# Kernel optimization log

Hardware: AMD Instinct MI355X
Metric: run time of the kernel (lower is better)

The kernel has to match this reference:

```python
import jax, jax.numpy as jnp
import numpy as np

N_SRC, N_DST, E = 10000, 10000, 640000
S, T, O, H = 128, 128, 128, 4
D = O // H


def setup_inputs() -> dict:
    key = jax.random.key(0)
    ks = jax.random.split(key, 12)
    f = lambda k, shape, fan: jax.random.normal(k, shape, dtype=jnp.float32) / np.float32(np.sqrt(fan))
    return {
        "x_src": jax.random.normal(ks[0], (N_SRC, S), dtype=jnp.float32),
        "x_dst": jax.random.normal(ks[1], (N_DST, T), dtype=jnp.float32),
        "W_pred1": f(ks[2], (S, T), T),
        "b_pred1": jnp.zeros((S,), jnp.float32),
        "W_pred2": f(ks[3], (S, S), S),
        "b_pred2": jnp.zeros((S,), jnp.float32),
        "W_res": f(ks[4], (H * D, S), S),
        "W_src": f(ks[5], (H * D, S), S),
        "W_dst": f(ks[6], (H * D, T), T),
        "att_src": jax.random.normal(ks[7], (1, H, D), dtype=jnp.float32) * 0.01,
        "att_dst": jax.random.normal(ks[8], (1, H, D), dtype=jnp.float32) * 0.01,
        "W_self": f(ks[9], (H * D, T), T),
        "b_self": jnp.zeros((H * D,), jnp.float32),
        "edge_src": jax.random.randint(ks[10], (E,), 0, N_SRC),
        "edge_dst": jax.random.randint(ks[11], (E,), 0, N_DST),
        "num_dst": N_DST,
    }


def reference(x_src, x_dst, W_pred1, b_pred1, W_pred2, b_pred2, W_res, W_src, W_dst,
              att_src, att_dst, W_self, b_self, edge_src, edge_dst, num_dst):
    h, d = att_src.shape[1], att_src.shape[2]
    # residual prediction path: pred_mlp(x_dst) = Lin2(ReLU(Lin1(x_dst)))
    pred = jax.nn.relu(x_dst @ W_pred1.T + b_pred1) @ W_pred2.T + b_pred2  # [Ndst,S]
    residual = x_src[edge_src] - pred[edge_dst]                            # [E,S]
    # per-node attention logits (equivalent to gather-then-dot, cheaper)
    a_s = ((x_src @ W_src.T).reshape(-1, h, d) * att_src).sum(-1)          # [Nsrc,H]
    a_d = ((x_dst @ W_dst.T).reshape(-1, h, d) * att_dst).sum(-1)          # [Ndst,H]
    alpha = jax.nn.leaky_relu(a_s[edge_src] + a_d[edge_dst], 0.2)          # [E,H]
    # edge softmax over incoming edges of each destination node
    amax = jax.ops.segment_max(alpha, edge_dst, num_segments=num_dst)      # [Ndst,H]
    ex = jnp.exp(alpha - amax[edge_dst])
    denom = jax.ops.segment_sum(ex, edge_dst, num_segments=num_dst)
    alpha = ex / (denom[edge_dst] + 1e-16)                                 # [E,H]
    # attention-weighted aggregation of transformed residuals
    msg = (residual @ W_res.T).reshape(-1, h, d) * alpha[:, :, None]       # [E,H,D]
    agg = jax.ops.segment_sum(msg.reshape(-1, h * d), edge_dst, num_segments=num_dst)
    return agg + x_dst @ W_self.T + b_self                                 # [Ndst,H*D]
```

## Files before the change

kernel.cpp:

```cpp
#include <hip/hip_runtime.h>
#include <hip/hip_bf16.h>

#define LEAKY 0.2f
#define CAP 160
#define CAPB 8192
#define CHUNK 2048
#define GSTRIDE 32

#define FMA4(A, S, V) do { (A).x += (S)*(V).x; (A).y += (S)*(V).y; (A).z += (S)*(V).z; (A).w += (S)*(V).w; } while (0)

typedef __attribute__((ext_vector_type(8))) short bf16x8;
typedef __attribute__((ext_vector_type(4))) float f32x4;

struct GemmJob {
  const float* X; const float* W; const float* B; float* Y;
  int M; int relu; int bf16out;
  const float* vvec;
  float* aout;
};

__device__ __forceinline__ unsigned short f2bf(float f) {
  unsigned int u = __float_as_uint(f);
  u += 0x7FFFu + ((u >> 16) & 1u);
  return (unsigned short)(u >> 16);
}
__device__ __forceinline__ float bf2f(unsigned short h) {
  return __uint_as_float(((unsigned int)h) << 16);
}

__device__ __forceinline__ bf16x8 pack8(const float4& a, const float4& b) {
  bf16x8 r;
  r[0] = (short)__builtin_bit_cast(unsigned short, __float2bfloat16(a.x));
  r[1] = (short)__builtin_bit_cast(unsigned short, __float2bfloat16(a.y));
  r[2] = (short)__builtin_bit_cast(unsigned short, __float2bfloat16(a.z));
  r[3] = (short)__builtin_bit_cast(unsigned short, __float2bfloat16(a.w));
  r[4] = (short)__builtin_bit_cast(unsigned short, __float2bfloat16(b.x));
  r[5] = (short)__builtin_bit_cast(unsigned short, __float2bfloat16(b.y));
  r[6] = (short)__builtin_bit_cast(unsigned short, __float2bfloat16(b.z));
  r[7] = (short)__builtin_bit_cast(unsigned short, __float2bfloat16(b.w));
  return r;
}

__device__ __forceinline__ void gemm128_mfma(
    const float* __restrict__ X, const float* __restrict__ W,
    const float* __restrict__ B, float* __restrict__ Y,
    int M, int relu, int bf16out, int row0,
    const float* vvec, float* __restrict__ aout) {
  if (row0 >= M) return;
  const int tid = threadIdx.x;
  const int wv = tid >> 6;
  const int ln = tid & 63;
  const int lr = ln & 15;
  const int kg = ln >> 4;

  const f32x4 zero = {0.f, 0.f, 0.f, 0.f};
  f32x4 acc[2][8];
#pragma unroll
  for (int mt = 0; mt < 2; mt++)
#pragma unroll
    for (int nt = 0; nt < 8; nt++) acc[mt][nt] = zero;

  float4 av0 = make_float4(0.f, 0.f, 0.f, 0.f), av1 = av0;

  const int r0 = row0 + wv * 32 + lr;
  const int r1 = r0 + 16;
  const int rc0 = r0 < M ? r0 : M - 1;
  const int rc1 = r1 < M ? r1 : M - 1;
  const float* xp0 = X + (size_t)rc0 * 128 + kg * 8;
  const float* xp1 = X + (size_t)rc1 * 128 + kg * 8;
  const float* wp  = W + (size_t)lr * 128 + kg * 8;

#pragma unroll
  for (int k0 = 0; k0 < 128; k0 += 32) {
    float4 xa0 = *(const float4*)(xp0 + k0);
    float4 xb0 = *(const float4*)(xp0 + k0 + 4);
    float4 xa1 = *(const float4*)(xp1 + k0);
    float4 xb1 = *(const float4*)(xp1 + k0 + 4);
    bf16x8 a0 = pack8(xa0, xb0);
    bf16x8 a1 = pack8(xa1, xb1);
#pragma unroll
    for (int nt = 0; nt < 8; nt++) {
      const float* wq = wp + (size_t)nt * 16 * 128 + k0;
      bf16x8 bw = pack8(*(const float4*)wq, *(const float4*)(wq + 4));
      acc[0][nt] = __builtin_amdgcn_mfma_f32_16x16x32_bf16(a0, bw, acc[0][nt], 0, 0, 0);
      acc[1][nt] = __builtin_amdgcn_mfma_f32_16x16x32_bf16(a1, bw, acc[1][nt], 0, 0, 0);
    }
    if (vvec) {
      const float4* vv = (const float4*)vvec + (k0 + kg * 8);
#pragma unroll
      for (int j = 0; j < 4; j++) {
        float4 v4 = vv[j];
        float s0 = (j == 0) ? xa0.x : (j == 1) ? xa0.y : (j == 2) ? xa0.z : xa0.w;
        float s1 = (j == 0) ? xa1.x : (j == 1) ? xa1.y : (j == 2) ? xa1.z : xa1.w;
        FMA4(av0, s0, v4); FMA4(av1, s1, v4);
      }
#pragma unroll
      for (int j = 0; j < 4; j++) {
        float4 v4 = vv[4 + j];
        float s0 = (j == 0) ? xb0.x : (j == 1) ? xb0.y : (j == 2) ? xb0.z : xb0.w;
        float s1 = (j == 0) ? xb1.x : (j == 1) ? xb1.y : (j == 2) ? xb1.z : xb1.w;
        FMA4(av0, s0, v4); FMA4(av1, s1, v4);
      }
    }
  }

  if (vvec) {
    av0.x += __shfl_xor(av0.x, 16, 64); av0.y += __shfl_xor(av0.y, 16, 64);
    av0.z += __shfl_xor(av0.z, 16, 64); av0.w += __shfl_xor(av0.w, 16, 64);
    av0.x += __shfl_xor(av0.x, 32, 64); av0.y += __shfl_xor(av0.y, 32, 64);
    av0.z += __shfl_xor(av0.z, 32, 64); av0.w += __shfl_xor(av0.w, 32, 64);
    av1.x += __shfl_xor(av1.x, 16, 64); av1.y += __shfl_xor(av1.y, 16, 64);
    av1.z += __shfl_xor(av1.z, 16, 64); av1.w += __shfl_xor(av1.w, 16, 64);
    av1.x += __shfl_xor(av1.x, 32, 64); av1.y += __shfl_xor(av1.y, 32, 64);
    av1.z += __shfl_xor(av1.z, 32, 64); av1.w += __shfl_xor(av1.w, 32, 64);
    if (kg == 0) {
      if (r0 < M) *(float4*)(aout + (size_t)r0 * 4) = av0;
      if (r1 < M) *(float4*)(aout + (size_t)r1 * 4) = av1;
    }
  }

  float bv[8];
#pragma unroll
  for (int nt = 0; nt < 8; nt++) bv[nt] = B ? B[nt * 16 + lr] : 0.f;

  const int rbase = row0 + wv * 32 + kg * 4;
#pragma unroll
  for (int mt = 0; mt < 2; mt++) {
#pragma unroll
    for (int i = 0; i < 4; i++) {
      int r = rbase + mt * 16 + i;
      if (r >= M) continue;
      if (bf16out) {
        unsigned short* yb = (unsigned short*)Y + (size_t)r * 128 + lr;
#pragma unroll
        for (int nt = 0; nt < 8; nt++) {
          float o = acc[mt][nt][i] + bv[nt];
          if (relu) o = fmaxf(o, 0.f);
          yb[nt * 16] = f2bf(o);
        }
      } else {
        float* yp = Y + (size_t)r * 128 + lr;
#pragma unroll
        for (int nt = 0; nt < 8; nt++) {
          float o = acc[mt][nt][i] + bv[nt];
          if (relu) o = fmaxf(o, 0.f);
          yp[nt * 16] = o;
        }
      }
    }
  }
}

__global__ __launch_bounds__(256) void phase1(
    const float* __restrict__ Wsrc, const float* __restrict__ attsrc,
    const float* __restrict__ Wdst, const float* __restrict__ attdst,
    const float* __restrict__ W_res, const float* __restrict__ W2,
    const float* __restrict__ b2,
    GemmJob jA,
    float* __restrict__ v_src, float* __restrict__ v_dst,
    float* __restrict__ Wc, float* __restrict__ bc,
    const int* __restrict__ edge_src, const int* __restrict__ edge_dst,
    int* __restrict__ gcnt, int* __restrict__ bin,
    int E, int Nd, int NB, int GA, int Q1, int T1) {
  __shared__ __align__(16) int bsm[2 * CHUNK + 4 * CAP];
  int bx = blockIdx.x, tid = threadIdx.x;
  int u = (bx & 7) * Q1 + (bx >> 3);
  if (u >= T1) return;
  if (u == 0) {
    int which = tid >> 7, k = tid & 127;
    const float* W = which ? Wdst : Wsrc;
    const float* att = which ? attdst : attsrc;
    float* v = which ? v_dst : v_src;
    float s[4] = {0.f, 0.f, 0.f, 0.f};
#pragma unroll
    for (int h = 0; h < 4; h++)
      for (int d = 0; d < 32; d++)
        s[h] += W[(size_t)(h * 32 + d) * 128 + k] * att[h * 32 + d];
#pragma unroll
    for (int h = 0; h < 4; h++) v[k * 4 + h] = s[h];
  } else if (u == 1) {
    if (tid < 128) {
      float s = 0.f;
      for (int i = 0; i < 128; i++) s += W_res[(size_t)tid * 128 + i] * b2[i];
      bc[tid] = s;
    }
  } else if (u < 66) {
    int id = (u - 2) * 256 + tid;
    int o = id >> 7, j = id & 127;
    float s = 0.f;
    for (int i = 0; i < 128; i++) s += W_res[(size_t)o * 128 + i] * W2[(size_t)i * 128 + j];
    Wc[(size_t)o * 128 + j] = s;
  } else if (u < 66 + GA) {
    gemm128_mfma(jA.X, jA.W, jA.B, jA.Y, jA.M, jA.relu, jA.bf16out,
                 (u - 66) * 128, nullptr, nullptr);
  } else {
    int* pk      = bsm;
    int* lsorted = pk + CHUNK;
    int* hist    = lsorted + CHUNK;
    int* gbase   = hist + CAP;
    int* lstart  = gbase + CAP;
    int* lcur    = lstart + CAP;
    int e0 = (u - 66 - GA) * CHUNK;
    int n = E - e0; if (n > CHUNK) n = CHUNK;
    if (n <= 0) return;
    for (int i = tid; i < NB; i += 256) hist[i] = 0;
    __syncthreads();
    for (int i = tid; i < n; i += 256) {
      int s = edge_src[e0 + i], d = edge_dst[e0 + i];
      pk[i] = (s << 14) | d;
      atomicAdd(&hist[d >> 6], 1);
    }
    __syncthreads();
    for (int b = tid; b < NB; b += 256)
      gbase[b] = hist[b] ? atomicAdd(&gcnt[b * GSTRIDE], hist[b]) : 0;
    if (tid < 64) {
      int PB = (NB + 63) >> 6;
      int sl = 0;
      for (int k = 0; k < PB; k++) { int idx = tid * PB + k; if (idx < NB) sl += hist[idx]; }
      int incl = sl;
#pragma unroll
      for (int off = 1; off < 64; off <<= 1) {
        int tv = __shfl_up(incl, off, 64);
        if (tid >= off) incl += tv;
      }
      int run = incl - sl;
      for (int k = 0; k < PB; k++) {
        int idx = tid * PB + k;
        if (idx < NB) { lstart[idx] = run; lcur[idx] = run; run += hist[idx]; }
      }
    }
    __syncthreads();
    for (int i = tid; i < n; i += 256) {
      int p = pk[i];
      int b = (p & 16383) >> 6;
      lsorted[atomicAdd(&lcur[b], 1)] = p;
    }
    __syncthreads();
    for (int j = tid; j < n; j += 256) {
      int p = lsorted[j];
      int b = (p & 16383) >> 6;
      int off = gbase[b] + (j - lstart[b]);
      if (off < CAPB) bin[(size_t)b * CAPB + off] = p;
    }
  }
}

__global__ __launch_bounds__(256) void phase2(
    GemmJob j0, GemmJob j1, GemmJob j2,
    const int* __restrict__ gcnt, const int* __restrict__ bin,
    int* __restrict__ sorted_src, int* __restrict__ rstart, int* __restrict__ rend,
    int Nd, int G, int Q2, int T2) {
  __shared__ __align__(16) int ssm[CAPB + 192];
  int bx = blockIdx.x, tid = threadIdx.x;
  int u = (bx % 6) * Q2 + bx / 6;
  if (u >= T2) return;
  if (u < 3 * G) {
    GemmJob J = (u < G) ? j0 : (u < 2 * G) ? j1 : j2;
    gemm128_mfma(J.X, J.W, J.B, J.Y, J.M, J.relu, J.bf16out, (u % G) * 128, J.vvec, J.aout);
  } else {
    int b = u - 3 * G;
    int* lsorted = ssm;
    int* hist2   = lsorted + CAPB;
    int* lstart2 = hist2 + 64;
    int* lcur2   = lstart2 + 64;
    int cnt = gcnt[b * GSTRIDE]; if (cnt > CAPB) cnt = CAPB;
    size_t base = (size_t)b * CAPB;
    if (tid < 64) hist2[tid] = 0;
    __syncthreads();
    for (int i = tid; i < cnt; i += 256) atomicAdd(&hist2[bin[base + i] & 63], 1);
    __syncthreads();
    if (tid < 64) {
      int v = hist2[tid];
      int incl = v;
#pragma unroll
      for (int off = 1; off < 64; off <<= 1) {
        int tv = __shfl_up(incl, off, 64);
        if (tid >= off) incl += tv;
      }
      int st = incl - v;
      lstart2[tid] = st; lcur2[tid] = st;
      int dst = (b << 6) + tid;
      if (dst < Nd) {
        rstart[dst] = (int)base + st;
        rend[dst]   = (int)base + st + v;
      }
    }
    __syncthreads();
    for (int i = tid; i < cnt; i += 256) {
      int p = bin[base + i];
      lsorted[atomicAdd(&lcur2[p & 63], 1)] = p >> 14;
    }
    __syncthreads();
    for (int i = tid; i < cnt; i += 256)
      sorted_src[base + i] = lsorted[i];
  }
}

__global__ __launch_bounds__(256) void phase3(
    const int* __restrict__ rstart, const int* __restrict__ rend,
    const int* __restrict__ sorted_src,
    const float* __restrict__ a_s, const float* __restrict__ a_d,
    const unsigned short* __restrict__ u_src, const float* __restrict__ u_pred,
    const float* __restrict__ self_o, float* __restrict__ out, int Nd) {
  __shared__ float smem[1920];
  int bx = blockIdx.x, tid = threadIdx.x;
  int half = tid >> 7;
  int t = tid & 127;
  int dst = bx * 2 + half;
  if (dst >= Nd) return;

  float* wbuf  = smem + half * 640;
  int* srcbuf  = (int*)(smem + 1280) + half * 160;
  float4* red4 = (float4*)(smem + 1600);
  float4* redv = (float4*)(smem + 1616) + half * 32;
  float* inv_s = smem + 1872 + half * 4;
  float* sA_s  = smem + 1880 + half * 4;

  int start = rstart[dst];
  int deg = rend[dst] - start;
  float4 ad4 = *(const float4*)(a_d + (size_t)dst * 4);
  float s0 = 0.f, s1 = 0.f, s2 = 0.f, s3 = 0.f;
  for (int i = t; i < deg; i += 128) {
    int src = sorted_src[start + i];
    float4 as4 = *(const float4*)(a_s + (size_t)src * 4);
    float l0 = as4.x + ad4.x; l0 = l0 > 0.f ? l0 : LEAKY * l0;
    float l1 = as4.y + ad4.y; l1 = l1 > 0.f ? l1 : LEAKY * l1;
    float l2 = as4.z + ad4.z; l2 = l2 > 0.f ? l2 : LEAKY * l2;
    float l3 = as4.w + ad4.w; l3 = l3 > 0.f ? l3 : LEAKY * l3;
    float w0 = __expf(l0), w1 = __expf(l1), w2 = __expf(l2), w3 = __expf(l3);
    if (i < CAP) {
      wbuf[i * 4 + 0] = w0; wbuf[i * 4 + 1] = w1;
      wbuf[i * 4 + 2] = w2; wbuf[i * 4 + 3] = w3;
      srcbuf[i] = src;
    }
    s0 += w0; s1 += w1; s2 += w2; s3 += w3;
  }
  int wave = tid >> 6;
#pragma unroll
  for (int off = 32; off > 0; off >>= 1) {
    s0 += __shfl_xor(s0, off, 64);
    s1 += __shfl_xor(s1, off, 64);
    s2 += __shfl_xor(s2, off, 64);
    s3 += __shfl_xor(s3, off, 64);
  }
  if ((tid & 63) == 0) red4[wave] = make_float4(s0, s1, s2, s3);
  __syncthreads();
  if (t == 0) {
    float4 A = red4[half * 2], B = red4[half * 2 + 1];
    float dx = A.x + B.x, dy = A.y + B.y, dz = A.z + B.z, dw = A.w + B.w;
    inv_s[0] = 1.f / (dx + 1e-16f); sA_s[0] = dx * inv_s[0];
    inv_s[1] = 1.f / (dy + 1e-16f); sA_s[1] = dy * inv_s[1];
    inv_s[2] = 1.f / (dz + 1e-16f); sA_s[2] = dz * inv_s[2];
    inv_s[3] = 1.f / (dw + 1e-16f); sA_s[3] = dw * inv_s[3];
  }
  __syncthreads();

  int c4 = t & 31, rgrp = t >> 5, h = c4 >> 3;
  int coff = c4 * 4;
  float4 acc0 = make_float4(0.f,0.f,0.f,0.f), acc1 = acc0, acc2 = acc0, acc3 = acc0;
  int cap = deg < CAP ? deg : CAP;
  int i = rgrp;
  for (; i + 12 < cap; i += 16) {
    int sA = srcbuf[i], sB = srcbuf[i + 4], sC = srcbuf[i + 8], sD = srcbuf[i + 12];
    float wA = wbuf[i * 4 + h], wB = wbuf[(i + 4) * 4 + h];
    float wC = wbuf[(i + 8) * 4 + h], wD = wbuf[(i + 12) * 4 + h];
    ushort4 hA = *(const ushort4*)(u_src + (size_t)sA * 128 + coff);
    ushort4 hB = *(const ushort4*)(u_src + (size_t)sB * 128 + coff);
    ushort4 hC = *(const ushort4*)(u_src + (size_t)sC * 128 + coff);
    ushort4 hD = *(const ushort4*)(u_src + (size_t)sD * 128 + coff);
    float4 uA = make_float4(bf2f(hA.x), bf2f(hA.y), bf2f(hA.z), bf2f(hA.w));
    float4 uB = make_float4(bf2f(hB.x), bf2f(hB.y), bf2f(hB.z), bf2f(hB.w));
    float4 uC = make_float4(bf2f(hC.x), bf2f(hC.y), bf2f(hC.z), bf2f(hC.w));
    float4 uD = make_float4(bf2f(hD.x), bf2f(hD.y), bf2f(hD.z), bf2f(hD.w));
    FMA4(acc0, wA, uA); FMA4(acc1, wB, uB); FMA4(acc2, wC, uC); FMA4(acc3, wD, uD);
  }
  for (; i < cap; i += 4) {
    int s_ = srcbuf[i];
    float w = wbuf[i * 4 + h];
    ushort4 hh = *(const ushort4*)(u_src + (size_t)s_ * 128 + coff);
    float4 uu = make_float4(bf2f(hh.x), bf2f(hh.y), bf2f(hh.z), bf2f(hh.w));
    FMA4(acc0, w, uu);
  }
  if (deg > CAP) {
    float adh = (h == 0) ? ad4.x : (h == 1) ? ad4.y : (h == 2) ? ad4.z : ad4.w;
    for (int k = CAP + rgrp; k < deg; k += 4) {
      int src = sorted_src[start + k];
      float l = a_s[(size_t)src * 4 + h] + adh;
      l = l > 0.f ? l : LEAKY * l;
      float w = __expf(l);
      ushort4 hh = *(const ushort4*)(u_src + (size_t)src * 128 + coff);
      float4 uu = make_float4(bf2f(hh.x), bf2f(hh.y), bf2f(hh.z), bf2f(hh.w));
      FMA4(acc0, w, uu);
    }
  }
  float4 acc;
  acc.x = acc0.x + acc1.x + acc2.x + acc3.x;
  acc.y = acc0.y + acc1.y + acc2.y + acc3.y;
  acc.z = acc0.z + acc1.z + acc2.z + acc3.z;
  acc.w = acc0.w + acc1.w + acc2.w + acc3.w;
  acc.x += __shfl_xor(acc.x, 32, 64);
  acc.y += __shfl_xor(acc.y, 32, 64);
  acc.z += __shfl_xor(acc.z, 32, 64);
  acc.w += __shfl_xor(acc.w, 32, 64);
  if (t >= 64 && t < 96) redv[c4] = acc;
  __syncthreads();
  if (t < 32) {
    float4 r = redv[c4];
    acc.x += r.x; acc.y += r.y; acc.z += r.z; acc.w += r.w;
    float4 up = *(const float4*)(u_pred + (size_t)dst * 128 + coff);
    float4 so = *(const float4*)(self_o + (size_t)dst * 128 + coff);
    float iv = inv_s[h], sa = sA_s[h];
    float4 o;
    o.x = acc.x * iv - sa * up.x + so.x;
    o.y = acc.y * iv - sa * up.y + so.y;
    o.z = acc.z * iv - sa * up.z + so.z;
    o.w = acc.w * iv - sa * up.w + so.w;
    *(float4*)(out + (size_t)dst * 128 + coff) = o;
  }
}

extern "C" void kernel_launch(void* const* d_in, const int* in_sizes, int n_in,
                              void* d_out, int out_size, void* d_ws, size_t ws_size,
                              hipStream_t stream) {
  const float* x_src   = (const float*)d_in[0];
  const float* x_dst   = (const float*)d_in[1];
  const float* W_pred1 = (const float*)d_in[2];
  const float* b_pred1 = (const float*)d_in[3];
  const float* W_pred2 = (const float*)d_in[4];
  const float* b_pred2 = (const float*)d_in[5];
  const float* W_res   = (const float*)d_in[6];
  const float* W_src   = (const float*)d_in[7];
  const float* W_dst   = (const float*)d_in[8];
  const float* att_src = (const float*)d_in[9];
  const float* att_dst = (const float*)d_in[10];
  const float* W_self  = (const float*)d_in[11];
  const float* b_self  = (const float*)d_in[12];
  const int* edge_src  = (const int*)d_in[13];
  const int* edge_dst  = (const int*)d_in[14];
  int Ns = in_sizes[0] / 128;
  int Nd = in_sizes[1] / 128;
  int E  = in_sizes[13];
  float* out = (float*)d_out;
  int NB = (Nd + 63) >> 6;

  char* ws = (char*)d_ws;
  auto alloc = [&](size_t bytes) -> char* {
    char* p = ws;
    ws += (bytes + 255) & ~(size_t)255;
    return p;
  };
  float* relu1  = (float*)alloc((size_t)Nd * 128 * 4);
  unsigned short* u_src = (unsigned short*)alloc((size_t)Ns * 128 * 2);
  float* u_pred = (float*)alloc((size_t)Nd * 128 * 4);
  float* self_o = (float*)alloc((size_t)Nd * 128 * 4);
  float* a_s    = (float*)alloc((size_t)Ns * 4 * 4);
  float* a_d    = (float*)alloc((size_t)Nd * 4 * 4);
  float* v_src  = (float*)alloc(128 * 4 * 4);
  float* v_dst  = (float*)alloc(128 * 4 * 4);
  float* Wc     = (float*)alloc(128 * 128 * 4);
  float* bc     = (float*)alloc(128 * 4);
  int* gcnt     = (int*)alloc((size_t)NB * GSTRIDE * 4);
  int* rstart   = (int*)alloc((size_t)Nd * 4);
  int* rend     = (int*)alloc((size_t)Nd * 4);
  int* bin      = (int*)alloc((size_t)NB * CAPB * 4);
  int* sorted_src = (int*)alloc((size_t)NB * CAPB * 4);

  hipMemsetAsync(gcnt, 0, (size_t)NB * GSTRIDE * sizeof(int), stream);

  int GA  = (Nd + 127) / 128;
  int NCH = (E + CHUNK - 1) / CHUNK;
  int T1 = 66 + GA + NCH;
  int Q1 = (T1 + 7) / 8;
  GemmJob jA{ x_dst, W_pred1, b_pred1, relu1, Nd, 1, 0, nullptr, nullptr };
  hipLaunchKernelGGL(phase1, dim3(Q1 * 8), dim3(256), 0, stream,
                     W_src, att_src, W_dst, att_dst, W_res, W_pred2, b_pred2, jA,
                     v_src, v_dst, Wc, bc, edge_src, edge_dst, gcnt, bin,
                     E, Nd, NB, GA, Q1, T1);

  int maxM = Ns > Nd ? Ns : Nd;
  int G  = (maxM + 127) / 128;
  int T2 = 3 * G + NB;
  int Q2 = (T2 + 5) / 6;
  GemmJob jB{ x_src, W_res,  nullptr, (float*)u_src, Ns, 0, 1, v_src, a_s };
  GemmJob jC{ x_dst, W_self, b_self,  self_o, Nd, 0, 0, v_dst, a_d };
  GemmJob jU{ relu1, Wc,     bc,      u_pred, Nd, 0, 0, nullptr, nullptr };
  hipLaunchKernelGGL(phase2, dim3(Q2 * 6), dim3(256), 0, stream,
                     jB, jC, jU, gcnt, bin, sorted_src, rstart, rend,
                     Nd, G, Q2, T2);

  hipLaunchKernelGGL(phase3, dim3((Nd + 1) / 2), dim3(256), 0, stream,
                     rstart, rend, sorted_src, a_s, a_d, u_src, u_pred, self_o, out, Nd);
}
```

Before: 158.7 us.

## Move attention-logit GEMMs into phase1 and shrink GEMM tiles to 64 rows

Moves the x_src·W_res and x_dst·W_self GEMMs, which also produce the attention logits, from phase2 into phase1. There they run alongside the edge binning and the first MLP layer, leaving phase2 with only the pred GEMM and the per-bucket sort. Each GEMM block now builds its own attention projection vectors in shared memory, so the separate v_src/v_dst producer block and its cross-kernel dependency are gone. The MFMA GEMM tile is halved to 64 rows per block, which doubles block count and lowers register pressure. In exchange, the projection vectors are recomputed redundantly in every block and each W tile is reused across fewer rows.

```diff
diff --git a/kernel.cpp b/kernel.cpp
--- a/kernel.cpp
+++ b/kernel.cpp
@@ -15,7 +15,8 @@
 struct GemmJob {
   const float* X; const float* W; const float* B; float* Y;
   int M; int relu; int bf16out;
-  const float* vvec;
+  const float* Wv;
+  const float* attv;
   float* aout;
 };
 
@@ -41,7 +42,7 @@
   return r;
 }
 
-__device__ __forceinline__ void gemm128_mfma(
+__device__ __forceinline__ void gemm64_mfma(
     const float* __restrict__ X, const float* __restrict__ W,
     const float* __restrict__ B, float* __restrict__ Y,
     int M, int relu, int bf16out, int row0,
@@ -54,36 +55,27 @@
   const int kg = ln >> 4;
 
   const f32x4 zero = {0.f, 0.f, 0.f, 0.f};
-  f32x4 acc[2][8];
-#pragma unroll
-  for (int mt = 0; mt < 2; mt++)
-#pragma unroll
-    for (int nt = 0; nt < 8; nt++) acc[mt][nt] = zero;
-
-  float4 av0 = make_float4(0.f, 0.f, 0.f, 0.f), av1 = av0;
-
-  const int r0 = row0 + wv * 32 + lr;
-  const int r1 = r0 + 16;
+  f32x4 acc[8];
+#pragma unroll
+  for (int nt = 0; nt < 8; nt++) acc[nt] = zero;
+
+  float4 av0 = make_float4(0.f, 0.f, 0.f, 0.f);
+
+  const int r0 = row0 + wv * 16 + lr;
   const int rc0 = r0 < M ? r0 : M - 1;
-  const int rc1 = r1 < M ? r1 : M - 1;
   const float* xp0 = X + (size_t)rc0 * 128 + kg * 8;
-  const float* xp1 = X + (size_t)rc1 * 128 + kg * 8;
   const float* wp  = W + (size_t)lr * 128 + kg * 8;
 
 #pragma unroll
   for (int k0 = 0; k0 < 128; k0 += 32) {
     float4 xa0 = *(const float4*)(xp0 + k0);
     float4 xb0 = *(const float4*)(xp0 + k0 + 4);
-    float4 xa1 = *(const float4*)(xp1 + k0);
-    float4 xb1 = *(const float4*)(xp1 + k0 + 4);
     bf16x8 a0 = pack8(xa0, xb0);
-    bf16x8 a1 = pack8(xa1, xb1);
 #pragma unroll
     for (int nt = 0; nt < 8; nt++) {
       const float* wq = wp + (size_t)nt * 16 * 128 + k0;
       bf16x8 bw = pack8(*(const float4*)wq, *(const float4*)(wq + 4));
-      acc[0][nt] = __builtin_amdgcn_mfma_f32_16x16x32_bf16(a0, bw, acc[0][nt], 0, 0, 0);
-      acc[1][nt] = __builtin_amdgcn_mfma_f32_16x16x32_bf16(a1, bw, acc[1][nt], 0, 0, 0);
+      acc[nt] = __builtin_amdgcn_mfma_f32_16x16x32_bf16(a0, bw, acc[nt], 0, 0, 0);
     }
     if (vvec) {
       const float4* vv = (const float4*)vvec + (k0 + kg * 8);
@@ -91,15 +83,13 @@
       for (int j = 0; j < 4; j++) {
         float4 v4 = vv[j];
         float s0 = (j == 0) ? xa0.x : (j == 1) ? xa0.y : (j == 2) ? xa0.z : xa0.w;
-        float s1 = (j == 0) ? xa1.x : (j == 1) ? xa1.y : (j == 2) ? xa1.z : xa1.w;
-        FMA4(av0, s0, v4); FMA4(av1, s1, v4);
+        FMA4(av0, s0, v4);
       }
 #pragma unroll
       for (int j = 0; j < 4; j++) {
         float4 v4 = vv[4 + j];
         float s0 = (j == 0) ? xb0.x : (j == 1) ? xb0.y : (j == 2) ? xb0.z : xb0.w;
-        float s1 = (j == 0) ? xb1.x : (j == 1) ? xb1.y : (j == 2) ? xb1.z : xb1.w;
-        FMA4(av0, s0, v4); FMA4(av1, s1, v4);
+        FMA4(av0, s0, v4);
       }
     }
   }
@@ -109,90 +99,87 @@
     av0.z += __shfl_xor(av0.z, 16, 64); av0.w += __shfl_xor(av0.w, 16, 64);
     av0.x += __shfl_xor(av0.x, 32, 64); av0.y += __shfl_xor(av0.y, 32, 64);
     av0.z += __shfl_xor(av0.z, 32, 64); av0.w += __shfl_xor(av0.w, 32, 64);
-    av1.x += __shfl_xor(av1.x, 16, 64); av1.y += __shfl_xor(av1.y, 16, 64);
-    av1.z += __shfl_xor(av1.z, 16, 64); av1.w += __shfl_xor(av1.w, 16, 64);
-    av1.x += __shfl_xor(av1.x, 32, 64); av1.y += __shfl_xor(av1.y, 32, 64);
-    av1.z += __shfl_xor(av1.z, 32, 64); av1.w += __shfl_xor(av1.w, 32, 64);
-    if (kg == 0) {
-      if (r0 < M) *(float4*)(aout + (size_t)r0 * 4) = av0;
-      if (r1 < M) *(float4*)(aout + (size_t)r1 * 4) = av1;
-    }
+    if (kg == 0 && r0 < M) *(float4*)(aout + (size_t)r0 * 4) = av0;
   }
 
   float bv[8];
 #pragma unroll
   for (int nt = 0; nt < 8; nt++) bv[nt] = B ? B[nt * 16 + lr] : 0.f;
 
-  const int rbase = row0 + wv * 32 + kg * 4;
-#pragma unroll
-  for (int mt = 0; mt < 2; mt++) {
-#pragma unroll
-    for (int i = 0; i < 4; i++) {
-      int r = rbase + mt * 16 + i;
-      if (r >= M) continue;
-      if (bf16out) {
-        unsigned short* yb = (unsigned short*)Y + (size_t)r * 128 + lr;
-#pragma unroll
-        for (int nt = 0; nt < 8; nt++) {
-          float o = acc[mt][nt][i] + bv[nt];
-          if (relu) o = fmaxf(o, 0.f);
-          yb[nt * 16] = f2bf(o);
-        }
-      } else {
-        float* yp = Y + (size_t)r * 128 + lr;
-#pragma unroll
-        for (int nt = 0; nt < 8; nt++) {
-          float o = acc[mt][nt][i] + bv[nt];
-          if (relu) o = fmaxf(o, 0.f);
-          yp[nt * 16] = o;
-        }
-      }
-    }
-  }
+  const int rbase = row0 + wv * 16 + kg * 4;
+#pragma unroll
+  for (int i = 0; i < 4; i++) {
+    int r = rbase + i;
+    if (r >= M) continue;
+    if (bf16out) {
+      unsigned short* yb = (unsigned short*)Y + (size_t)r * 128 + lr;
+#pragma unroll
+      for (int nt = 0; nt < 8; nt++) {
+        float o = acc[nt][i] + bv[nt];
+        if (relu) o = fmaxf(o, 0.f);
+        yb[nt * 16] = f2bf(o);
+      }
+    } else {
+      float* yp = Y + (size_t)r * 128 + lr;
+#pragma unroll
+      for (int nt = 0; nt < 8; nt++) {
+        float o = acc[nt][i] + bv[nt];
+        if (relu) o = fmaxf(o, 0.f);
+        yp[nt * 16] = o;
+      }
+    }
+  }
+}
+
+__device__ __forceinline__ void gemm_unit(const GemmJob& J, int row0, char* smemraw) {
+  const float* vvec = nullptr;
+  if (J.Wv) {
+    float* vl = (float*)smemraw;
+    for (int idx = threadIdx.x; idx < 512; idx += 256) {
+      int k = idx >> 2, h = idx & 3;
+      const float* wp = J.Wv + (size_t)(h * 32) * 128 + k;
+      const float* ap = J.attv + h * 32;
+      float s = 0.f;
+#pragma unroll 8
+      for (int d = 0; d < 32; d++) s += wp[(size_t)d * 128] * ap[d];
+      vl[idx] = s;
+    }
+    __syncthreads();
+    vvec = vl;
+  }
+  gemm64_mfma(J.X, J.W, J.B, J.Y, J.M, J.relu, J.bf16out, row0, vvec, J.aout);
 }
 
 __global__ __launch_bounds__(256) void phase1(
-    const float* __restrict__ Wsrc, const float* __restrict__ attsrc,
-    const float* __restrict__ Wdst, const float* __restrict__ attdst,
     const float* __restrict__ W_res, const float* __restrict__ W2,
     const float* __restrict__ b2,
-    GemmJob jA,
-    float* __restrict__ v_src, float* __restrict__ v_dst,
+    GemmJob jA, GemmJob jB, GemmJob jC,
     float* __restrict__ Wc, float* __restrict__ bc,
     const int* __restrict__ edge_src, const int* __restrict__ edge_dst,
     int* __restrict__ gcnt, int* __restrict__ bin,
-    int E, int Nd, int NB, int GA, int Q1, int T1) {
+    int E, int Nd, int NB, int GAd, int GBs, int Q1, int T1) {
   __shared__ __align__(16) int bsm[2 * CHUNK + 4 * CAP];
   int bx = blockIdx.x, tid = threadIdx.x;
   int u = (bx & 7) * Q1 + (bx >> 3);
   if (u >= T1) return;
-  if (u == 0) {
-    int which = tid >> 7, k = tid & 127;
-    const float* W = which ? Wdst : Wsrc;
-    const float* att = which ? attdst : attsrc;
-    float* v = which ? v_dst : v_src;
-    float s[4] = {0.f, 0.f, 0.f, 0.f};
-#pragma unroll
-    for (int h = 0; h < 4; h++)
-      for (int d = 0; d < 32; d++)
-        s[h] += W[(size_t)(h * 32 + d) * 128 + k] * att[h * 32 + d];
-#pragma unroll
-    for (int h = 0; h < 4; h++) v[k * 4 + h] = s[h];
-  } else if (u == 1) {
+  if (u < 64) {
+    int id = u * 256 + tid;
+    int o = id >> 7, j = id & 127;
+    float s = 0.f;
+    for (int i = 0; i < 128; i++) s += W_res[(size_t)o * 128 + i] * W2[(size_t)i * 128 + j];
+    Wc[(size_t)o * 128 + j] = s;
+  } else if (u == 64) {
     if (tid < 128) {
       float s = 0.f;
       for (int i = 0; i < 128; i++) s += W_res[(size_t)tid * 128 + i] * b2[i];
       bc[tid] = s;
     }
-  } else if (u < 66) {
-    int id = (u - 2) * 256 + tid;
-    int o = id >> 7, j = id & 127;
-    float s = 0.f;
-    for (int i = 0; i < 128; i++) s += W_res[(size_t)o * 128 + i] * W2[(size_t)i * 128 + j];
-    Wc[(size_t)o * 128 + j] = s;
-  } else if (u < 66 + GA) {
-    gemm128_mfma(jA.X, jA.W, jA.B, jA.Y, jA.M, jA.relu, jA.bf16out,
-                 (u - 66) * 128, nullptr, nullptr);
+  } else if (u < 65 + GAd) {
+    gemm_unit(jA, (u - 65) * 64, (char*)bsm);
+  } else if (u < 65 + GAd + GBs) {
+    gemm_unit(jB, (u - 65 - GAd) * 64, (char*)bsm);
+  } else if (u < 65 + GAd + GBs + GAd) {
+    gemm_unit(jC, (u - 65 - GAd - GBs) * 64, (char*)bsm);
   } else {
     int* pk      = bsm;
     int* lsorted = pk + CHUNK;
@@ -200,7 +187,7 @@
     int* gbase   = hist + CAP;
     int* lstart  = gbase + CAP;
     int* lcur    = lstart + CAP;
-    int e0 = (u - 66 - GA) * CHUNK;
+    int e0 = (u - (65 + 2 * GAd + GBs)) * CHUNK;
     int n = E - e0; if (n > CHUNK) n = CHUNK;
     if (n <= 0) return;
     for (int i = tid; i < NB; i += 256) hist[i] = 0;
@@ -246,19 +233,18 @@
 }
 
 __global__ __launch_bounds__(256) void phase2(
-    GemmJob j0, GemmJob j1, GemmJob j2,
+    GemmJob jU,
     const int* __restrict__ gcnt, const int* __restrict__ bin,
     int* __restrict__ sorted_src, int* __restrict__ rstart, int* __restrict__ rend,
-    int Nd, int G, int Q2, int T2) {
+    int Nd, int GUd, int Q2, int T2) {
   __shared__ __align__(16) int ssm[CAPB + 192];
   int bx = blockIdx.x, tid = threadIdx.x;
   int u = (bx % 6) * Q2 + bx / 6;
   if (u >= T2) return;
-  if (u < 3 * G) {
-    GemmJob J = (u < G) ? j0 : (u < 2 * G) ? j1 : j2;
-    gemm128_mfma(J.X, J.W, J.B, J.Y, J.M, J.relu, J.bf16out, (u % G) * 128, J.vvec, J.aout);
+  if (u < GUd) {
+    gemm64_mfma(jU.X, jU.W, jU.B, jU.Y, jU.M, jU.relu, jU.bf16out, u * 64, nullptr, nullptr);
   } else {
-    int b = u - 3 * G;
+    int b = u - GUd;
     int* lsorted = ssm;
     int* hist2   = lsorted + CAPB;
     int* lstart2 = hist2 + 64;
@@ -455,8 +441,6 @@
   float* self_o = (float*)alloc((size_t)Nd * 128 * 4);
   float* a_s    = (float*)alloc((size_t)Ns * 4 * 4);
   float* a_d    = (float*)alloc((size_t)Nd * 4 * 4);
-  float* v_src  = (float*)alloc(128 * 4 * 4);
-  float* v_dst  = (float*)alloc(128 * 4 * 4);
   float* Wc     = (float*)alloc(128 * 128 * 4);
   float* bc     = (float*)alloc(128 * 4);
   int* gcnt     = (int*)alloc((size_t)NB * GSTRIDE * 4);
@@ -467,26 +451,27 @@
 
   hipMemsetAsync(gcnt, 0, (size_t)NB * GSTRIDE * sizeof(int), stream);
 
-  int GA  = (Nd + 127) / 128;
+  int GAd = (Nd + 63) / 64;
+  int GBs = (Ns + 63) / 64;
   int NCH = (E + CHUNK - 1) / CHUNK;
-  int T1 = 66 + GA + NCH;
+
+  GemmJob jA{ x_dst, W_pred1, b_pred1, relu1, Nd, 1, 0, nullptr, nullptr, nullptr };
+  GemmJob jB{ x_src, W_res,  nullptr, (float*)u_src, Ns, 0, 1, W_src, att_src, a_s };
+  GemmJob jC{ x_dst, W_self, b_self,  self_o, Nd, 0, 0, W_dst, att_dst, a_d };
+  GemmJob jU{ relu1, Wc,     bc,      u_pred, Nd, 0, 0, nullptr, nullptr, nullptr };
+
+  int T1 = 65 + 2 * GAd + GBs + NCH;
   int Q1 = (T1 + 7) / 8;
-  GemmJob jA{ x_dst, W_pred1, b_pred1, relu1, Nd, 1, 0, nullptr, nullptr };
   hipLaunchKernelGGL(phase1, dim3(Q1 * 8), dim3(256), 0, stream,
-                     W_src, att_src, W_dst, att_dst, W_res, W_pred2, b_pred2, jA,
-                     v_src, v_dst, Wc, bc, edge_src, edge_dst, gcnt, bin,
-                     E, Nd, NB, GA, Q1, T1);
-
-  int maxM = Ns > Nd ? Ns : Nd;
-  int G  = (maxM + 127) / 128;
-  int T2 = 3 * G + NB;
+                     W_res, W_pred2, b_pred2, jA, jB, jC, Wc, bc,
+                     edge_src, edge_dst, gcnt, bin,
+                     E, Nd, NB, GAd, GBs, Q1, T1);
+
+  int T2 = GAd + NB;
   int Q2 = (T2 + 5) / 6;
-  GemmJob jB{ x_src, W_res,  nullptr, (float*)u_src, Ns, 0, 1, v_src, a_s };
-  GemmJob jC{ x_dst, W_self, b_self,  self_o, Nd, 0, 0, v_dst, a_d };
-  GemmJob jU{ relu1, Wc,     bc,      u_pred, Nd, 0, 0, nullptr, nullptr };
   hipLaunchKernelGGL(phase2, dim3(Q2 * 6), dim3(256), 0, stream,
-                     jB, jC, jU, gcnt, bin, sorted_src, rstart, rend,
-                     Nd, G, Q2, T2);
+                     jU, gcnt, bin, sorted_src, rstart, rend,
+                     Nd, GAd, Q2, T2);
 
   hipLaunchKernelGGL(phase3, dim3((Nd + 1) / 2), dim3(256), 0, stream,
                      rstart, rend, sorted_src, a_s, a_d, u_src, u_pred, self_o, out, Nd);
```

New measurement: 180.9 us. 1.14x slower.

## Fuse pred MLP and W_res projection into one chained per-tile GEMM unit

Applied to the files above, without the earlier changes.

Replaces the precomputed combined weight Wc = W_res·W2 and the separate relu1 GEMM with one phase1 unit per 128-row tile. That unit runs three chained MFMA GEMMs (W1+ReLU, W2, W_res) and keeps the bf16 intermediates in swizzled LDS. This removes the relu1 global round trip, the Wc/bc setup blocks and the third GEMM job from phase2, shortening the critical path. In exchange it does one extra 128x128 GEMM per tile, adds extra bf16 rounding of intermediates, and makes phase1 GEMM units much heavier than the binning units.

```diff
diff --git a/kernel.cpp b/kernel.cpp
--- a/kernel.cpp
+++ b/kernel.cpp
@@ -151,18 +151,124 @@
   }
 }
 
+__device__ __forceinline__ void stage_acc_lds(
+    unsigned short* __restrict__ T, const f32x4 acc[2][8],
+    const float* __restrict__ bias, int relu, int wv, int lr, int kg) {
+  float bv[8];
+#pragma unroll
+  for (int nt = 0; nt < 8; nt++) bv[nt] = bias ? bias[nt * 16 + lr] : 0.f;
+#pragma unroll
+  for (int mt = 0; mt < 2; mt++)
+#pragma unroll
+    for (int i = 0; i < 4; i++) {
+      int r = wv * 32 + mt * 16 + kg * 4 + i;
+      int sw = (r & 7) << 3;
+#pragma unroll
+      for (int nt = 0; nt < 8; nt++) {
+        int c = nt * 16 + lr;
+        float o = acc[mt][nt][i] + bv[nt];
+        if (relu) o = fmaxf(o, 0.f);
+        T[(r * 128 + c) ^ sw] = f2bf(o);
+      }
+    }
+}
+
+__device__ __forceinline__ void gemm128_ldsA(
+    const unsigned short* __restrict__ T, const float* __restrict__ W,
+    f32x4 acc[2][8], int wv, int lr, int kg) {
+  const int r0 = wv * 32 + lr, r1 = r0 + 16;
+  const int sw = (lr & 7) << 3;
+  const float* wp = W + (size_t)lr * 128 + kg * 8;
+#pragma unroll
+  for (int k0 = 0; k0 < 128; k0 += 32) {
+    bf16x8 a0 = *(const bf16x8*)(T + ((r0 * 128 + k0 + kg * 8) ^ sw));
+    bf16x8 a1 = *(const bf16x8*)(T + ((r1 * 128 + k0 + kg * 8) ^ sw));
+#pragma unroll
+    for (int nt = 0; nt < 8; nt++) {
+      const float* wq = wp + (size_t)nt * 16 * 128 + k0;
+      bf16x8 bw = pack8(*(const float4*)wq, *(const float4*)(wq + 4));
+      acc[0][nt] = __builtin_amdgcn_mfma_f32_16x16x32_bf16(a0, bw, acc[0][nt], 0, 0, 0);
+      acc[1][nt] = __builtin_amdgcn_mfma_f32_16x16x32_bf16(a1, bw, acc[1][nt], 0, 0, 0);
+    }
+  }
+}
+
+__device__ __forceinline__ void jau_unit(
+    const float* __restrict__ X, const float* __restrict__ W1, const float* __restrict__ b1,
+    const float* __restrict__ W2, const float* __restrict__ b2,
+    const float* __restrict__ Wr, float* __restrict__ Y,
+    int M, int row0, unsigned short* __restrict__ T) {
+  if (row0 >= M) return;
+  const int tid = threadIdx.x;
+  const int wv = tid >> 6, ln = tid & 63, lr = ln & 15, kg = ln >> 4;
+  const f32x4 zero = {0.f, 0.f, 0.f, 0.f};
+  f32x4 acc[2][8];
+
+#pragma unroll
+  for (int mt = 0; mt < 2; mt++)
+#pragma unroll
+    for (int nt = 0; nt < 8; nt++) acc[mt][nt] = zero;
+  {
+    const int r0 = row0 + wv * 32 + lr, r1 = r0 + 16;
+    const int rc0 = r0 < M ? r0 : M - 1, rc1 = r1 < M ? r1 : M - 1;
+    const float* xp0 = X + (size_t)rc0 * 128 + kg * 8;
+    const float* xp1 = X + (size_t)rc1 * 128 + kg * 8;
+    const float* wp  = W1 + (size_t)lr * 128 + kg * 8;
+#pragma unroll
+    for (int k0 = 0; k0 < 128; k0 += 32) {
+      bf16x8 a0 = pack8(*(const float4*)(xp0 + k0), *(const float4*)(xp0 + k0 + 4));
+      bf16x8 a1 = pack8(*(const float4*)(xp1 + k0), *(const float4*)(xp1 + k0 + 4));
+#pragma unroll
+      for (int nt = 0; nt < 8; nt++) {
+        const float* wq = wp + (size_t)nt * 16 * 128 + k0;
+        bf16x8 bw = pack8(*(const float4*)wq, *(const float4*)(wq + 4));
+        acc[0][nt] = __builtin_amdgcn_mfma_f32_16x16x32_bf16(a0, bw, acc[0][nt], 0, 0, 0);
+        acc[1][nt] = __builtin_amdgcn_mfma_f32_16x16x32_bf16(a1, bw, acc[1][nt], 0, 0, 0);
+      }
+    }
+  }
+  stage_acc_lds(T, acc, b1, 1, wv, lr, kg);
+  __syncthreads();
+
+#pragma unroll
+  for (int mt = 0; mt < 2; mt++)
+#pragma unroll
+    for (int nt = 0; nt < 8; nt++) acc[mt][nt] = zero;
+  gemm128_ldsA(T, W2, acc, wv, lr, kg);
+  __syncthreads();
+  stage_acc_lds(T, acc, b2, 0, wv, lr, kg);
+  __syncthreads();
+
+#pragma unroll
+  for (int mt = 0; mt < 2; mt++)
+#pragma unroll
+    for (int nt = 0; nt < 8; nt++) acc[mt][nt] = zero;
+  gemm128_ldsA(T, Wr, acc, wv, lr, kg);
+  const int rbase = row0 + wv * 32 + kg * 4;
+#pragma unroll
+  for (int mt = 0; mt < 2; mt++)
+#pragma unroll
+    for (int i = 0; i < 4; i++) {
+      int r = rbase + mt * 16 + i;
+      if (r >= M) continue;
+      float* yp = Y + (size_t)r * 128 + lr;
+#pragma unroll
+      for (int nt = 0; nt < 8; nt++) yp[nt * 16] = acc[mt][nt][i];
+    }
+}
+
 __global__ __launch_bounds__(256) void phase1(
     const float* __restrict__ Wsrc, const float* __restrict__ attsrc,
     const float* __restrict__ Wdst, const float* __restrict__ attdst,
-    const float* __restrict__ W_res, const float* __restrict__ W2,
-    const float* __restrict__ b2,
-    GemmJob jA,
+    const float* __restrict__ x_dst, const float* __restrict__ W1,
+    const float* __restrict__ b1, const float* __restrict__ W2,
+    const float* __restrict__ b2, const float* __restrict__ W_res,
+    float* __restrict__ u_pred,
     float* __restrict__ v_src, float* __restrict__ v_dst,
-    float* __restrict__ Wc, float* __restrict__ bc,
     const int* __restrict__ edge_src, const int* __restrict__ edge_dst,
     int* __restrict__ gcnt, int* __restrict__ bin,
-    int E, int Nd, int NB, int GA, int Q1, int T1) {
-  __shared__ __align__(16) int bsm[2 * CHUNK + 4 * CAP];
+    int E, int Nd, int NB, int GAd, int Q1, int T1) {
+  __shared__ __align__(16) char smemraw[32768];
   int bx = blockIdx.x, tid = threadIdx.x;
   int u = (bx & 7) * Q1 + (bx >> 3);
   if (u >= T1) return;
@@ -178,29 +284,18 @@
         s[h] += W[(size_t)(h * 32 + d) * 128 + k] * att[h * 32 + d];
 #pragma unroll
     for (int h = 0; h < 4; h++) v[k * 4 + h] = s[h];
-  } else if (u == 1) {
-    if (tid < 128) {
-      float s = 0.f;
-      for (int i = 0; i < 128; i++) s += W_res[(size_t)tid * 128 + i] * b2[i];
-      bc[tid] = s;
-    }
-  } else if (u < 66) {
-    int id = (u - 2) * 256 + tid;
-    int o = id >> 7, j = id & 127;
-    float s = 0.f;
-    for (int i = 0; i < 128; i++) s += W_res[(size_t)o * 128 + i] * W2[(size_t)i * 128 + j];
-    Wc[(size_t)o * 128 + j] = s;
-  } else if (u < 66 + GA) {
-    gemm128_mfma(jA.X, jA.W, jA.B, jA.Y, jA.M, jA.relu, jA.bf16out,
-                 (u - 66) * 128, nullptr, nullptr);
+  } else if (u < 1 + GAd) {
+    jau_unit(x_dst, W1, b1, W2, b2, W_res, u_pred, Nd, (u - 1) * 128,
+             (unsigned short*)smemraw);
   } else {
+    int* bsm     = (int*)smemraw;
     int* pk      = bsm;
     int* lsorted = pk + CHUNK;
     int* hist    = lsorted + CHUNK;
     int* gbase   = hist + CAP;
     int* lstart  = gbase + CAP;
     int* lcur    = lstart + CAP;
-    int e0 = (u - 66 - GA) * CHUNK;
+    int e0 = (u - 1 - GAd) * CHUNK;
     int n = E - e0; if (n > CHUNK) n = CHUNK;
     if (n <= 0) return;
     for (int i = tid; i < NB; i += 256) hist[i] = 0;
@@ -246,7 +341,7 @@
 }
 
 __global__ __launch_bounds__(256) void phase2(
-    GemmJob j0, GemmJob j1, GemmJob j2,
+    GemmJob j0, GemmJob j1,
     const int* __restrict__ gcnt, const int* __restrict__ bin,
     int* __restrict__ sorted_src, int* __restrict__ rstart, int* __restrict__ rend,
     int Nd, int G, int Q2, int T2) {
@@ -254,11 +349,11 @@
   int bx = blockIdx.x, tid = threadIdx.x;
   int u = (bx % 6) * Q2 + bx / 6;
   if (u >= T2) return;
-  if (u < 3 * G) {
-    GemmJob J = (u < G) ? j0 : (u < 2 * G) ? j1 : j2;
+  if (u < 2 * G) {
+    GemmJob J = (u < G) ? j0 : j1;
     gemm128_mfma(J.X, J.W, J.B, J.Y, J.M, J.relu, J.bf16out, (u % G) * 128, J.vvec, J.aout);
   } else {
-    int b = u - 3 * G;
+    int b = u - 2 * G;
     int* lsorted = ssm;
     int* hist2   = lsorted + CAPB;
     int* lstart2 = hist2 + 64;
@@ -449,7 +544,6 @@
     ws += (bytes + 255) & ~(size_t)255;
     return p;
   };
-  float* relu1  = (float*)alloc((size_t)Nd * 128 * 4);
   unsigned short* u_src = (unsigned short*)alloc((size_t)Ns * 128 * 2);
   float* u_pred = (float*)alloc((size_t)Nd * 128 * 4);
   float* self_o = (float*)alloc((size_t)Nd * 128 * 4);
@@ -457,8 +551,6 @@
   float* a_d    = (float*)alloc((size_t)Nd * 4 * 4);
   float* v_src  = (float*)alloc(128 * 4 * 4);
   float* v_dst  = (float*)alloc(128 * 4 * 4);
-  float* Wc     = (float*)alloc(128 * 128 * 4);
-  float* bc     = (float*)alloc(128 * 4);
   int* gcnt     = (int*)alloc((size_t)NB * GSTRIDE * 4);
   int* rstart   = (int*)alloc((size_t)Nd * 4);
   int* rend     = (int*)alloc((size_t)Nd * 4);
@@ -467,25 +559,25 @@
 
   hipMemsetAsync(gcnt, 0, (size_t)NB * GSTRIDE * sizeof(int), stream);
 
-  int GA  = (Nd + 127) / 128;
+  int GAd = (Nd + 127) / 128;
   int NCH = (E + CHUNK - 1) / CHUNK;
-  int T1 = 66 + GA + NCH;
+
+  int T1 = 1 + GAd + NCH;
   int Q1 = (T1 + 7) / 8;
-  GemmJob jA{ x_dst, W_pred1, b_pred1, relu1, Nd, 1, 0, nullptr, nullptr };
   hipLaunchKernelGGL(phase1, dim3(Q1 * 8), dim3(256), 0, stream,
-                     W_src, att_src, W_dst, att_dst, W_res, W_pred2, b_pred2, jA,
-                     v_src, v_dst, Wc, bc, edge_src, edge_dst, gcnt, bin,
-                     E, Nd, NB, GA, Q1, T1);
+                     W_src, att_src, W_dst, att_dst,
+                     x_dst, W_pred1, b_pred1, W_pred2, b_pred2, W_res, u_pred,
+                     v_src, v_dst, edge_src, edge_dst, gcnt, bin,
+                     E, Nd, NB, GAd, Q1, T1);
 
   int maxM = Ns > Nd ? Ns : Nd;
   int G  = (maxM + 127) / 128;
-  int T2 = 3 * G + NB;
+  int T2 = 2 * G + NB;
   int Q2 = (T2 + 5) / 6;
   GemmJob jB{ x_src, W_res,  nullptr, (float*)u_src, Ns, 0, 1, v_src, a_s };
   GemmJob jC{ x_dst, W_self, b_self,  self_o, Nd, 0, 0, v_dst, a_d };
-  GemmJob jU{ relu1, Wc,     bc,      u_pred, Nd, 0, 0, nullptr, nullptr };
   hipLaunchKernelGGL(phase2, dim3(Q2 * 6), dim3(256), 0, stream,
-                     jB, jC, jU, gcnt, bin, sorted_src, rstart, rend,
+                     jB, jC, gcnt, bin, sorted_src, rstart, rend,
                      Nd, G, Q2, T2);
 
   hipLaunchKernelGGL(phase3, dim3((Nd + 1) / 2), dim3(256), 0, stream,
```

Measured after the change: 186.9 us. +17.8%, slower.

## Fuse pred second-layer GEMM into phase3 as per-node matvec

Applied to the files above, without the earlier changes.

Removes the relu1·Wc GEMM job from phase2 and instead computes each destination's u_pred row inside phase3, with a per-thread 128-long dot product against Wc using the relu1 row staged in shared memory. This drops one third of the phase2 GEMM tiles and the u_pred write and read round trip through global memory. In exchange phase3 does scalar FP32 work of 128x128 FMAs per node, where the MFMA path was used before. It also reads a full Wc row per thread (strided across threads) and adds an extra barrier and more shared memory, which may lower occupancy.

```diff
diff --git a/kernel.cpp b/kernel.cpp
--- a/kernel.cpp
+++ b/kernel.cpp
@@ -246,7 +246,7 @@
 }
 
 __global__ __launch_bounds__(256) void phase2(
-    GemmJob j0, GemmJob j1, GemmJob j2,
+    GemmJob j0, GemmJob j1,
     const int* __restrict__ gcnt, const int* __restrict__ bin,
     int* __restrict__ sorted_src, int* __restrict__ rstart, int* __restrict__ rend,
     int Nd, int G, int Q2, int T2) {
@@ -254,11 +254,11 @@
   int bx = blockIdx.x, tid = threadIdx.x;
   int u = (bx % 6) * Q2 + bx / 6;
   if (u >= T2) return;
-  if (u < 3 * G) {
-    GemmJob J = (u < G) ? j0 : (u < 2 * G) ? j1 : j2;
+  if (u < 2 * G) {
+    GemmJob J = (u < G) ? j0 : j1;
     gemm128_mfma(J.X, J.W, J.B, J.Y, J.M, J.relu, J.bf16out, (u % G) * 128, J.vvec, J.aout);
   } else {
-    int b = u - 3 * G;
+    int b = u - 2 * G;
     int* lsorted = ssm;
     int* hist2   = lsorted + CAPB;
     int* lstart2 = hist2 + 64;
@@ -300,21 +300,39 @@
     const int* __restrict__ rstart, const int* __restrict__ rend,
     const int* __restrict__ sorted_src,
     const float* __restrict__ a_s, const float* __restrict__ a_d,
-    const unsigned short* __restrict__ u_src, const float* __restrict__ u_pred,
+    const unsigned short* __restrict__ u_src,
+    const float* __restrict__ relu1, const float* __restrict__ Wc,
+    const float* __restrict__ bc,
     const float* __restrict__ self_o, float* __restrict__ out, int Nd) {
-  __shared__ float smem[1920];
+  __shared__ float smem[2400];
   int bx = blockIdx.x, tid = threadIdx.x;
   int half = tid >> 7;
   int t = tid & 127;
   int dst = bx * 2 + half;
   if (dst >= Nd) return;
 
-  float* wbuf  = smem + half * 640;
-  int* srcbuf  = (int*)(smem + 1280) + half * 160;
-  float4* red4 = (float4*)(smem + 1600);
-  float4* redv = (float4*)(smem + 1616) + half * 32;
-  float* inv_s = smem + 1872 + half * 4;
-  float* sA_s  = smem + 1880 + half * 4;
+  float* wbuf    = smem + half * 640;
+  int* srcbuf    = (int*)(smem + 1280) + half * 160;
+  float* relu_l  = smem + 1600 + half * 128;
+  float* upred_l = smem + 1856 + half * 128;
+  float4* red4   = (float4*)(smem + 2112);
+  float4* redv   = (float4*)(smem + 2128) + half * 32;
+  float* inv_s   = smem + 2384 + half * 4;
+  float* sA_s    = smem + 2392 + half * 4;
+
+  relu_l[t] = relu1[(size_t)dst * 128 + t];
+  __syncthreads();
+  {
+    float s = bc[t];
+    const float4* wr = (const float4*)(Wc + (size_t)t * 128);
+    const float4* rl = (const float4*)relu_l;
+#pragma unroll 8
+    for (int k = 0; k < 32; k++) {
+      float4 w4 = wr[k], r4 = rl[k];
+      s += r4.x * w4.x + r4.y * w4.y + r4.z * w4.z + r4.w * w4.w;
+    }
+    upred_l[t] = s;
+  }
 
   int start = rstart[dst];
   int deg = rend[dst] - start;
@@ -407,7 +425,7 @@
   if (t < 32) {
     float4 r = redv[c4];
     acc.x += r.x; acc.y += r.y; acc.z += r.z; acc.w += r.w;
-    float4 up = *(const float4*)(u_pred + (size_t)dst * 128 + coff);
+    float4 up = make_float4(upred_l[coff], upred_l[coff + 1], upred_l[coff + 2], upred_l[coff + 3]);
     float4 so = *(const float4*)(self_o + (size_t)dst * 128 + coff);
     float iv = inv_s[h], sa = sA_s[h];
     float4 o;
@@ -451,7 +469,6 @@
   };
   float* relu1  = (float*)alloc((size_t)Nd * 128 * 4);
   unsigned short* u_src = (unsigned short*)alloc((size_t)Ns * 128 * 2);
-  float* u_pred = (float*)alloc((size_t)Nd * 128 * 4);
   float* self_o = (float*)alloc((size_t)Nd * 128 * 4);
   float* a_s    = (float*)alloc((size_t)Ns * 4 * 4);
   float* a_d    = (float*)alloc((size_t)Nd * 4 * 4);
@@ -479,15 +496,15 @@
 
   int maxM = Ns > Nd ? Ns : Nd;
   int G  = (maxM + 127) / 128;
-  int T2 = 3 * G + NB;
+  int T2 = 2 * G + NB;
   int Q2 = (T2 + 5) / 6;
   GemmJob jB{ x_src, W_res,  nullptr, (float*)u_src, Ns, 0, 1, v_src, a_s };
   GemmJob jC{ x_dst, W_self, b_self,  self_o, Nd, 0, 0, v_dst, a_d };
-  GemmJob jU{ relu1, Wc,     bc,      u_pred, Nd, 0, 0, nullptr, nullptr };
   hipLaunchKernelGGL(phase2, dim3(Q2 * 6), dim3(256), 0, stream,
-                     jB, jC, jU, gcnt, bin, sorted_src, rstart, rend,
+                     jB, jC, gcnt, bin, sorted_src, rstart, rend,
                      Nd, G, Q2, T2);
 
   hipLaunchKernelGGL(phase3, dim3((Nd + 1) / 2), dim3(256), 0, stream,
-                     rstart, rend, sorted_src, a_s, a_d, u_src, u_pred, self_o, out, Nd);
-}
+                     rstart, rend, sorted_src, a_s, a_d, u_src,
+                     relu1, Wc, bc, self_o, out, Nd);
+}
```

Result: slower. 222.9 us (+40.5%).
